# Optimization experiments

Measured on AMD Instinct MI355X. Metric: run time of the kernel, lower is better.

The kernel has to match this reference:

```python
import jax, jax.numpy as jnp
import numpy as np

N = 30000        # nodes
E = 480000       # edges
IN_DIM = 128
HID = 64
OUT = 64
POS_DIM = 32
H = 4            # heads (same for all layers)
PVOCAB = 3
NEG_SLOPE = 0.2


def _xavier(key, shape):
    fan_in, fan_out = shape[0], shape[-1] if len(shape) > 1 else shape[0]
    scale = 1.414 * np.sqrt(2.0 / (fan_in + fan_out))
    return jax.random.normal(key, shape, dtype=jnp.float32) * scale


def setup_inputs() -> dict:
    key = jax.random.key(0)
    ks = jax.random.split(key, 20)
    d0_in = IN_DIM + POS_DIM            # 160
    d_mid = HID * H + POS_DIM           # 288
    inp = {
        "features": jax.random.normal(ks[0], (N, IN_DIM), dtype=jnp.float32),
        # layer 0
        "W0": _xavier(ks[1], (d0_in, H * HID)),
        "al0": _xavier(ks[2], (H, HID)),
        "ar0": _xavier(ks[3], (H, HID)),
        "pe0": _xavier(ks[4], (PVOCAB, POS_DIM)),
        # layer 1
        "W1": _xavier(ks[5], (d_mid, H * HID)),
        "al1": _xavier(ks[6], (H, HID)),
        "ar1": _xavier(ks[7], (H, HID)),
        "pe1": _xavier(ks[8], (PVOCAB, POS_DIM)),
        # output layer
        "W2": _xavier(ks[9], (d_mid, H * OUT)),
        "al2": _xavier(ks[10], (H, OUT)),
        "ar2": _xavier(ks[11], (H, OUT)),
        "pe2": _xavier(ks[12], (PVOCAB, POS_DIM)),
        # graph
        "src": jax.random.randint(ks[13], (E,), 0, N, dtype=jnp.int32),
        "dst": jax.random.randint(ks[14], (E,), 0, N, dtype=jnp.int32),
        "pos": jax.random.randint(ks[15], (N,), 0, PVOCAB, dtype=jnp.int32),
    }
    return inp


def gat_layer(h, W, a_l, a_r, src, dst):
    # h: [N, in_d]; W: [in_d, H*d]; a_l,a_r: [H, d]
    n = h.shape[0]
    nh, d = a_l.shape
    ft = (h @ W).reshape(n, nh, d)                       # [N,H,d]
    a1 = jnp.einsum("nhd,hd->nh", ft, a_l)               # [N,H]
    a2 = jnp.einsum("nhd,hd->nh", ft, a_r)               # [N,H]
    e = jax.nn.leaky_relu(a1[src] + a2[dst], NEG_SLOPE)  # [E,H]
    # per-destination segment softmax (numerically stable)
    m = jax.ops.segment_max(e, dst, num_segments=n)      # [N,H]
    ex = jnp.exp(e - m[dst])                             # [E,H]
    s = jax.ops.segment_sum(ex, dst, num_segments=n)     # [N,H]
    alpha = ex / s[dst]                                  # [E,H]
    msg = ft[src] * alpha[:, :, None]                    # [E,H,d]
    return jax.ops.segment_sum(msg, dst, num_segments=n) # [N,H,d]


def reference(features, W0, al0, ar0, pe0, W1, al1, ar1, pe1,
              W2, al2, ar2, pe2, src, dst, pos):
    h = features
    # hidden GAT layers with ELU activation and head-flattening
    for W, al, ar, pe in ((W0, al0, ar0, pe0), (W1, al1, ar1, pe1)):
        p = pe[pos]                                      # [N, pos_dim]
        hcat = jnp.concatenate((h, p), axis=1)
        out = gat_layer(hcat, W, al, ar, src, dst)       # [N,H,d]
        h = jax.nn.elu(out.reshape(out.shape[0], -1))    # [N,H*d]
    # output layer: mean over heads
    p = pe2[pos]
    hcat = jnp.concatenate((h, p), axis=1)
    out = gat_layer(hcat, W2, al2, ar2, src, dst)        # [N,H,out]
    return out.mean(axis=1)                              # [N,out]
```

## Files before the change

### kernel.cpp

```cpp
#include <hip/hip_runtime.h>
#include <hip/hip_fp16.h>
#include <math.h>

#define N_NODES 30000
#define N_EDGES 480000
#define HEADS 4
#define DHEAD 64
#define FDIM 256
#define POSD 32
#define CAPB 96
#define HIST_NB 1875
#define G0_NB 940

typedef _Float16 half8 __attribute__((ext_vector_type(8)));
typedef float floatx4 __attribute__((ext_vector_type(4)));

__device__ __forceinline__ float lrelu(float x){ return x > 0.f ? x : 0.2f * x; }

struct h16 { __half2 a, b, c, d; };
union hu { half8 v; h16 s; };

template<typename T>
__device__ __forceinline__ void gemm_body(
    int bx, int by, const T* __restrict__ A, const _Float16* __restrict__ Wt,
    const float* __restrict__ PW, const int* __restrict__ pos,
    const float* __restrict__ al, const float* __restrict__ arw,
    _Float16* __restrict__ Ch, float* __restrict__ a1, float* __restrict__ a2,
    int K){
  int t = threadIdx.x;
  int w = t >> 6;
  int lane = t & 63;
  int lm = lane & 15;
  int kq = lane >> 4;
  int h = bx;
  int rowBase = by * 128 + w * 32;
  int colBase = h * DHEAD;

  floatx4 acc[2][4] = {};

  const T* Ar[2];
#pragma unroll
  for (int r = 0; r < 2; r++)
    Ar[r] = A + (size_t)min(rowBase + r * 16 + lm, N_NODES - 1) * K;
  const _Float16* Bp[4];
#pragma unroll
  for (int j = 0; j < 4; j++)
    Bp[j] = Wt + (size_t)(colBase + j * 16 + lm) * K;

  for (int kb = 0; kb < K; kb += 32){
    int ko = kb + kq * 8;
    half8 bf[4];
#pragma unroll
    for (int j = 0; j < 4; j++) bf[j] = *(const half8*)(Bp[j] + ko);
#pragma unroll
    for (int r = 0; r < 2; r++){
      half8 af;
      if constexpr (sizeof(T) == 2){
        af = *(const half8*)(Ar[r] + ko);
      } else {
        float4 u0 = *(const float4*)(Ar[r] + ko);
        float4 u1 = *(const float4*)(Ar[r] + ko + 4);
        af[0] = (_Float16)u0.x; af[1] = (_Float16)u0.y;
        af[2] = (_Float16)u0.z; af[3] = (_Float16)u0.w;
        af[4] = (_Float16)u1.x; af[5] = (_Float16)u1.y;
        af[6] = (_Float16)u1.z; af[7] = (_Float16)u1.w;
      }
#pragma unroll
      for (int j = 0; j < 4; j++)
        acc[r][j] = __builtin_amdgcn_mfma_f32_16x16x32_f16(af, bf[j], acc[r][j], 0, 0, 0);
    }
  }

  float alw[4], arr[4];
#pragma unroll
  for (int j = 0; j < 4; j++){
    int col = j * 16 + lm;
    alw[j] = al [h * DHEAD + col];
    arr[j] = arw[h * DHEAD + col];
  }

#pragma unroll
  for (int r = 0; r < 2; r++){
#pragma unroll
    for (int p = 0; p < 4; p++){
      int row = rowBase + r * 16 + kq * 4 + p;
      if (row < N_NODES){
        int pz = pos[row];
        const float* pwb = PW + pz * FDIM + colBase;
        float s1 = 0.f, s2 = 0.f;
#pragma unroll
        for (int j = 0; j < 4; j++){
          float v = acc[r][j][p] + pwb[j * 16 + lm];
          Ch[(size_t)row * FDIM + colBase + j * 16 + lm] = (_Float16)v;
          s1 = fmaf(v, alw[j], s1);
          s2 = fmaf(v, arr[j], s2);
        }
#pragma unroll
        for (int o2 = 1; o2 <= 8; o2 <<= 1){
          s1 += __shfl_xor(s1, o2, 64);
          s2 += __shfl_xor(s2, o2, 64);
        }
        if (lm == 0){
          a1[row * HEADS + h] = s1;
          a2[row * HEADS + h] = s2;
        }
      }
    }
  }
}

__device__ __forceinline__ void pair_batch(
    const _Float16* __restrict__ ftp, int sr, float wr, int base,
    int eh, int hh, float4& aL, float4& aH){
  int s4[4]; float w4[4]; hu f4[4];
#pragma unroll
  for (int u = 0; u < 4; u++){
    int eu = base + 2 * u + eh;
    s4[u] = __shfl(sr, eu, 64);
    w4[u] = __shfl(wr, eu | (hh << 4), 64);
  }
#pragma unroll
  for (int u = 0; u < 4; u++)
    f4[u].v = *(const half8*)(ftp + (size_t)s4[u] * FDIM);
#pragma unroll
  for (int u = 0; u < 4; u++){
    float2 p0 = __half22float2(f4[u].s.a);
    float2 p1 = __half22float2(f4[u].s.b);
    float2 p2 = __half22float2(f4[u].s.c);
    float2 p3 = __half22float2(f4[u].s.d);
    float wu = w4[u];
    aL.x = fmaf(wu, p0.x, aL.x); aL.y = fmaf(wu, p0.y, aL.y);
    aL.z = fmaf(wu, p1.x, aL.z); aL.w = fmaf(wu, p1.y, aL.w);
    aH.x = fmaf(wu, p2.x, aH.x); aH.y = fmaf(wu, p2.y, aH.y);
    aH.z = fmaf(wu, p3.x, aH.z); aH.w = fmaf(wu, p3.y, aH.w);
  }
}

__device__ __forceinline__ void agg_node(
    int n, const _Float16* __restrict__ ft, const float* __restrict__ a1,
    const float* __restrict__ a2, const int* __restrict__ degv,
    const int* __restrict__ esrc, int lane, float4& aL, float4& aH){
  int jb = n * CAPB;
  int deg = min(degv[n], CAPB);
  int eidx = lane & 15, h = lane >> 4;
  int eh = lane >> 5;
  int c8 = lane & 31;
  int hh = (lane >> 3) & 3;
  float a2n = a2[n * HEADS + h];
  aL = make_float4(0.f, 0.f, 0.f, 0.f);
  aH = make_float4(0.f, 0.f, 0.f, 0.f);
  const _Float16* ftp = ft + (size_t)c8 * 8;

  if (deg <= 64){
    int sreg[4];
#pragma unroll
    for (int r = 0; r < 4; r++){
      int idx = eidx + r * 16;
      sreg[r] = (idx < deg) ? esrc[jb + idx] : 0;
    }
    float av[4];
#pragma unroll
    for (int r = 0; r < 4; r++)
      av[r] = a1[sreg[r] * HEADS + h];
    int sA[4]; hu fA[4];
#pragma unroll
    for (int u = 0; u < 4; u++) sA[u] = __shfl(sreg[0], 2 * u + eh, 64);
#pragma unroll
    for (int u = 0; u < 4; u++)
      fA[u].v = *(const half8*)(ftp + (size_t)sA[u] * FDIM);

    float wreg[4];
    float m = -INFINITY;
#pragma unroll
    for (int r = 0; r < 4; r++){
      int idx = eidx + r * 16;
      float e = (idx < deg) ? lrelu(av[r] + a2n) : -INFINITY;
      wreg[r] = e;
      m = fmaxf(m, e);
    }
    m = fmaxf(m, __shfl_xor(m, 1, 64));
    m = fmaxf(m, __shfl_xor(m, 2, 64));
    m = fmaxf(m, __shfl_xor(m, 4, 64));
    m = fmaxf(m, __shfl_xor(m, 8, 64));
    float ss = 0.f;
#pragma unroll
    for (int r = 0; r < 4; r++){
      int idx = eidx + r * 16;
      float tv = (idx < deg) ? __expf(wreg[r] - m) : 0.f;
      wreg[r] = tv;
      ss += tv;
    }
    ss += __shfl_xor(ss, 1, 64);
    ss += __shfl_xor(ss, 2, 64);
    ss += __shfl_xor(ss, 4, 64);
    ss += __shfl_xor(ss, 8, 64);
    float inv = (ss > 0.f) ? 1.f / ss : 0.f;
#pragma unroll
    for (int r = 0; r < 4; r++) wreg[r] *= inv;

    {
      float w4[4];
#pragma unroll
      for (int u = 0; u < 4; u++)
        w4[u] = __shfl(wreg[0], (2 * u + eh) | (hh << 4), 64);
#pragma unroll
      for (int u = 0; u < 4; u++){
        float2 p0 = __half22float2(fA[u].s.a);
        float2 p1 = __half22float2(fA[u].s.b);
        float2 p2 = __half22float2(fA[u].s.c);
        float2 p3 = __half22float2(fA[u].s.d);
        float wu = w4[u];
        aL.x = fmaf(wu, p0.x, aL.x); aL.y = fmaf(wu, p0.y, aL.y);
        aL.z = fmaf(wu, p1.x, aL.z); aL.w = fmaf(wu, p1.y, aL.w);
        aH.x = fmaf(wu, p2.x, aH.x); aH.y = fmaf(wu, p2.y, aH.y);
        aH.z = fmaf(wu, p3.x, aH.z); aH.w = fmaf(wu, p3.y, aH.w);
      }
    }
    if (deg > 8)
      pair_batch(ftp, sreg[0], wreg[0], 8, eh, hh, aL, aH);
#pragma unroll
    for (int r = 1; r < 4; r++){
      if (r * 16 >= deg) break;
      pair_batch(ftp, sreg[r], wreg[r], 0, eh, hh, aL, aH);
      if (deg > r * 16 + 8)
        pair_batch(ftp, sreg[r], wreg[r], 8, eh, hh, aL, aH);
    }
  } else {
    float m = -INFINITY;
    for (int idx = eidx; idx < deg; idx += 16){
      int s = esrc[jb + idx];
      m = fmaxf(m, lrelu(a1[s * HEADS + h] + a2n));
    }
    m = fmaxf(m, __shfl_xor(m, 1, 64));
    m = fmaxf(m, __shfl_xor(m, 2, 64));
    m = fmaxf(m, __shfl_xor(m, 4, 64));
    m = fmaxf(m, __shfl_xor(m, 8, 64));
    float ss = 0.f;
    for (int idx = eidx; idx < deg; idx += 16){
      int s = esrc[jb + idx];
      ss += __expf(lrelu(a1[s * HEADS + h] + a2n) - m);
    }
    ss += __shfl_xor(ss, 1, 64);
    ss += __shfl_xor(ss, 2, 64);
    ss += __shfl_xor(ss, 4, 64);
    ss += __shfl_xor(ss, 8, 64);
    float inv = (ss > 0.f) ? 1.f / ss : 0.f;
    float m2  = __shfl(m,   hh << 4, 64);
    float iv2 = __shfl(inv, hh << 4, 64);
    float a2h = __shfl(a2n, hh << 4, 64);
    for (int j = eh; j < deg; j += 2){
      int sj = esrc[jb + j];
      float e = lrelu(a1[sj * HEADS + hh] + a2h);
      float wj = __expf(e - m2) * iv2;
      hu f; f.v = *(const half8*)(ftp + (size_t)sj * FDIM);
      float2 p0 = __half22float2(f.s.a);
      float2 p1 = __half22float2(f.s.b);
      float2 p2 = __half22float2(f.s.c);
      float2 p3 = __half22float2(f.s.d);
      aL.x = fmaf(wj, p0.x, aL.x); aL.y = fmaf(wj, p0.y, aL.y);
      aL.z = fmaf(wj, p1.x, aL.z); aL.w = fmaf(wj, p1.y, aL.w);
      aH.x = fmaf(wj, p2.x, aH.x); aH.y = fmaf(wj, p2.y, aH.y);
      aH.z = fmaf(wj, p3.x, aH.z); aH.w = fmaf(wj, p3.y, aH.w);
    }
  }
}

__global__ __launch_bounds__(256) void agg4_k(
    const _Float16* __restrict__ ft, const float* __restrict__ a1,
    const float* __restrict__ a2, const int* __restrict__ degv,
    const int* __restrict__ esrc, _Float16* __restrict__ outh,
    float* __restrict__ outf, int mode){
  int wv = threadIdx.x >> 6;
  int lane = threadIdx.x & 63;
  int n = blockIdx.x * 4 + wv;
  if (n >= N_NODES) return;
  float4 aL, aH;
  agg_node(n, ft, a1, a2, degv, esrc, lane, aL, aH);

  aL.x += __shfl_xor(aL.x, 32, 64); aL.y += __shfl_xor(aL.y, 32, 64);
  aL.z += __shfl_xor(aL.z, 32, 64); aL.w += __shfl_xor(aL.w, 32, 64);
  aH.x += __shfl_xor(aH.x, 32, 64); aH.y += __shfl_xor(aH.y, 32, 64);
  aH.z += __shfl_xor(aH.z, 32, 64); aH.w += __shfl_xor(aH.w, 32, 64);

  if (mode == 0){
    aL.x = aL.x > 0.f ? aL.x : (__expf(aL.x) - 1.f);
    aL.y = aL.y > 0.f ? aL.y : (__expf(aL.y) - 1.f);
    aL.z = aL.z > 0.f ? aL.z : (__expf(aL.z) - 1.f);
    aL.w = aL.w > 0.f ? aL.w : (__expf(aL.w) - 1.f);
    aH.x = aH.x > 0.f ? aH.x : (__expf(aH.x) - 1.f);
    aH.y = aH.y > 0.f ? aH.y : (__expf(aH.y) - 1.f);
    aH.z = aH.z > 0.f ? aH.z : (__expf(aH.z) - 1.f);
    aH.w = aH.w > 0.f ? aH.w : (__expf(aH.w) - 1.f);
    if (lane < 32){
      h16 o;
      o.a = __float22half2_rn(make_float2(aL.x, aL.y));
      o.b = __float22half2_rn(make_float2(aL.z, aL.w));
      o.c = __float22half2_rn(make_float2(aH.x, aH.y));
      o.d = __float22half2_rn(make_float2(aH.z, aH.w));
      *(h16*)&outh[(size_t)n * FDIM + (size_t)lane * 8] = o;
    }
  } else {
#pragma unroll
    for (int o2 = 8; o2 <= 16; o2 <<= 1){
      aL.x += __shfl_xor(aL.x, o2, 64); aL.y += __shfl_xor(aL.y, o2, 64);
      aL.z += __shfl_xor(aL.z, o2, 64); aL.w += __shfl_xor(aL.w, o2, 64);
      aH.x += __shfl_xor(aH.x, o2, 64); aH.y += __shfl_xor(aH.y, o2, 64);
      aH.z += __shfl_xor(aH.z, o2, 64); aH.w += __shfl_xor(aH.w, o2, 64);
    }
    if (lane < 8){
      float4 o0 = make_float4(aL.x * 0.25f, aL.y * 0.25f,
                              aL.z * 0.25f, aL.w * 0.25f);
      float4 o1 = make_float4(aH.x * 0.25f, aH.y * 0.25f,
                              aH.z * 0.25f, aH.w * 0.25f);
      *(float4*)&outf[(size_t)n * DHEAD + (size_t)lane * 8]     = o0;
      *(float4*)&outf[(size_t)n * DHEAD + (size_t)lane * 8 + 4] = o1;
    }
  }
}

__global__ __launch_bounds__(256) void prep0_k(
    const float* __restrict__ W0, const float* __restrict__ pe0,
    _Float16* __restrict__ T0, float* __restrict__ PW, int* __restrict__ deg){
  int blk = blockIdx.x, n = threadIdx.x;
  if (blk < 64){
    for (int k = blk; k < 128; k += 64)
      T0[(size_t)n * 128 + k] = (_Float16)W0[(size_t)k * FDIM + n];
  } else if (blk < 67){
    int v = blk - 64;
    float s = 0.f;
#pragma unroll
    for (int k = 0; k < POSD; k++)
      s = fmaf(pe0[v * POSD + k], W0[(size_t)(128 + k) * FDIM + n], s);
    PW[v * FDIM + n] = s;
  } else {
    int i = (blk - 67) * 256 + n;
    if (i < N_NODES) deg[i] = 0;
  }
}

__global__ __launch_bounds__(256, 2) void fused0_k(
    const float* __restrict__ A, const _Float16* __restrict__ Wt0,
    const float* __restrict__ PW0, const int* __restrict__ pos,
    const float* __restrict__ al0, const float* __restrict__ ar0,
    _Float16* __restrict__ Ch, float* __restrict__ a1, float* __restrict__ a2,
    const int* __restrict__ src, const int* __restrict__ dst,
    int* __restrict__ deg, int* __restrict__ esrc,
    const float* __restrict__ W1, const float* __restrict__ W2,
    _Float16* __restrict__ T1, _Float16* __restrict__ T2,
    const float* __restrict__ pe1, const float* __restrict__ pe2,
    float* __restrict__ PWall){
  int blk = blockIdx.x;
  if (blk < G0_NB){
    gemm_body<float>(blk & 3, blk >> 2, A, Wt0, PW0, pos, al0, ar0,
                     Ch, a1, a2, 128);
  } else if (blk < G0_NB + HIST_NB){
    int e = (blk - G0_NB) * 256 + threadIdx.x;
    if (e < N_EDGES){
      int d = dst[e];
      int slot = atomicAdd(&deg[d], 1);
      if (slot < CAPB) esrc[d * CAPB + slot] = src[e];
    }
  } else if (blk < G0_NB + HIST_NB + 128){
    int q = blk - G0_NB - HIST_NB;
    int l = q >> 6, kk0 = q & 63;
    const float* W = l == 0 ? W1 : W2;
    _Float16* T    = l == 0 ? T1 : T2;
    int n = threadIdx.x;
    for (int k = kk0; k < 256; k += 64)
      T[(size_t)n * 256 + k] = (_Float16)W[(size_t)k * FDIM + n];
  } else {
    int q = blk - G0_NB - HIST_NB - 128;
    int layer = q / 3 + 1, v = q % 3;
    const float* W  = layer == 1 ? W1 : W2;
    const float* pe = layer == 1 ? pe1 : pe2;
    int j = threadIdx.x;
    float s = 0.f;
#pragma unroll
    for (int k = 0; k < POSD; k++)
      s = fmaf(pe[v * POSD + k], W[(size_t)(256 + k) * FDIM + j], s);
    PWall[(layer * 3 + v) * FDIM + j] = s;
  }
}

template<typename T>
__global__ __launch_bounds__(256, 2) void gemm_k(
    const T* __restrict__ A, const _Float16* __restrict__ Wt,
    const float* __restrict__ PW, const int* __restrict__ pos,
    const float* __restrict__ al, const float* __restrict__ arw,
    _Float16* __restrict__ Ch, float* __restrict__ a1, float* __restrict__ a2,
    int K){
  gemm_body<T>(blockIdx.x, blockIdx.y, A, Wt, PW, pos, al, arw, Ch, a1, a2, K);
}

extern "C" void kernel_launch(void* const* d_in, const int* in_sizes, int n_in,
                              void* d_out, int out_size, void* d_ws, size_t ws_size,
                              hipStream_t stream){
  const float* features = (const float*)d_in[0];
  const float* W0  = (const float*)d_in[1];
  const float* al0 = (const float*)d_in[2];
  const float* ar0 = (const float*)d_in[3];
  const float* pe0 = (const float*)d_in[4];
  const float* W1  = (const float*)d_in[5];
  const float* al1 = (const float*)d_in[6];
  const float* ar1 = (const float*)d_in[7];
  const float* pe1 = (const float*)d_in[8];
  const float* W2  = (const float*)d_in[9];
  const float* al2 = (const float*)d_in[10];
  const float* ar2 = (const float*)d_in[11];
  const float* pe2 = (const float*)d_in[12];
  const int* srcv  = (const int*)d_in[13];
  const int* dstv  = (const int*)d_in[14];
  const int* posv  = (const int*)d_in[15];
  float* out = (float*)d_out;

  char* wp = (char*)d_ws;
  auto alloc = [&](size_t bytes){
    void* q = (void*)wp;
    wp += (bytes + 255) & ~(size_t)255;
    return q;
  };
  _Float16* fth  = (_Float16*)alloc(sizeof(_Float16) * (size_t)N_NODES * FDIM);
  _Float16* hbuf = (_Float16*)alloc(sizeof(_Float16) * (size_t)N_NODES * FDIM);
  _Float16* Wt0  = (_Float16*)alloc(sizeof(_Float16) * 256 * 128);
  _Float16* Wt1  = (_Float16*)alloc(sizeof(_Float16) * 256 * 256);
  _Float16* Wt2  = (_Float16*)alloc(sizeof(_Float16) * 256 * 256);
  float* a1   = (float*)alloc(sizeof(float) * N_NODES * HEADS);
  float* a2   = (float*)alloc(sizeof(float) * N_NODES * HEADS);
  float* PW   = (float*)alloc(sizeof(float) * 9 * FDIM);
  int*   deg  = (int*)alloc(sizeof(int) * N_NODES);
  int*   esrc = (int*)alloc(sizeof(int) * (size_t)N_NODES * CAPB);

  prep0_k<<<185, 256, 0, stream>>>(W0, pe0, Wt0, PW, deg);

  fused0_k<<<G0_NB + HIST_NB + 134, 256, 0, stream>>>(
      features, Wt0, PW, posv, al0, ar0, fth, a1, a2,
      srcv, dstv, deg, esrc, W1, W2, Wt1, Wt2, pe1, pe2, PW);

  dim3 ggrid(4, (N_NODES + 127) / 128);
  int agrid = (N_NODES + 3) / 4;

  agg4_k<<<agrid, 256, 0, stream>>>(fth, a1, a2, deg, esrc, hbuf, nullptr, 0);

  gemm_k<_Float16><<<ggrid, 256, 0, stream>>>(
      hbuf, Wt1, PW + 3 * FDIM, posv, al1, ar1, fth, a1, a2, 256);
  agg4_k<<<agrid, 256, 0, stream>>>(fth, a1, a2, deg, esrc, hbuf, nullptr, 0);

  gemm_k<_Float16><<<ggrid, 256, 0, stream>>>(
      hbuf, Wt2, PW + 6 * FDIM, posv, al2, ar2, fth, a1, a2, 256);
  agg4_k<<<agrid, 256, 0, stream>>>(fth, a1, a2, deg, esrc, nullptr, out, 1);
}
```

Baseline: 284.2 us.

## Fuse hidden-layer aggregation with next layer's GEMM through shared memory

```diff
diff --git a/kernel.cpp b/kernel.cpp
--- a/kernel.cpp
+++ b/kernel.cpp
@@ -11,6 +11,7 @@
 #define CAPB 96
 #define HIST_NB 1875
 #define G0_NB 940
+#define LDS_STRIDE 264
 
 typedef _Float16 half8 __attribute__((ext_vector_type(8)));
 typedef float floatx4 __attribute__((ext_vector_type(4)));
@@ -265,11 +266,121 @@
   }
 }
 
+__global__ __launch_bounds__(256) void aggemm32_k(
+    const _Float16* __restrict__ ftin, const float* __restrict__ a1in,
+    const float* __restrict__ a2in, const int* __restrict__ degv,
+    const int* __restrict__ esrc, const _Float16* __restrict__ Wt,
+    const float* __restrict__ PW, const int* __restrict__ pos,
+    const float* __restrict__ al, const float* __restrict__ arw,
+    _Float16* __restrict__ ftout, float* __restrict__ a1out,
+    float* __restrict__ a2out){
+  __shared__ _Float16 As[32 * LDS_STRIDE];
+  int t = threadIdx.x;
+  int wv = t >> 6;
+  int lane = t & 63;
+  int rb = blockIdx.x * 32;
+
+  for (int i = 0; i < 8; i++){
+    int rl = wv * 8 + i;
+    int n = rb + rl;
+    float4 aL = make_float4(0.f, 0.f, 0.f, 0.f);
+    float4 aH = make_float4(0.f, 0.f, 0.f, 0.f);
+    if (n < N_NODES){
+      agg_node(n, ftin, a1in, a2in, degv, esrc, lane, aL, aH);
+      aL.x += __shfl_xor(aL.x, 32, 64); aL.y += __shfl_xor(aL.y, 32, 64);
+      aL.z += __shfl_xor(aL.z, 32, 64); aL.w += __shfl_xor(aL.w, 32, 64);
+      aH.x += __shfl_xor(aH.x, 32, 64); aH.y += __shfl_xor(aH.y, 32, 64);
+      aH.z += __shfl_xor(aH.z, 32, 64); aH.w += __shfl_xor(aH.w, 32, 64);
+      aL.x = aL.x > 0.f ? aL.x : (__expf(aL.x) - 1.f);
+      aL.y = aL.y > 0.f ? aL.y : (__expf(aL.y) - 1.f);
+      aL.z = aL.z > 0.f ? aL.z : (__expf(aL.z) - 1.f);
+      aL.w = aL.w > 0.f ? aL.w : (__expf(aL.w) - 1.f);
+      aH.x = aH.x > 0.f ? aH.x : (__expf(aH.x) - 1.f);
+      aH.y = aH.y > 0.f ? aH.y : (__expf(aH.y) - 1.f);
+      aH.z = aH.z > 0.f ? aH.z : (__expf(aH.z) - 1.f);
+      aH.w = aH.w > 0.f ? aH.w : (__expf(aH.w) - 1.f);
+    }
+    if (lane < 32){
+      h16 o;
+      o.a = __float22half2_rn(make_float2(aL.x, aL.y));
+      o.b = __float22half2_rn(make_float2(aL.z, aL.w));
+      o.c = __float22half2_rn(make_float2(aH.x, aH.y));
+      o.d = __float22half2_rn(make_float2(aH.z, aH.w));
+      *(h16*)&As[rl * LDS_STRIDE + lane * 8] = o;
+    }
+  }
+  __syncthreads();
+
+  int lm = lane & 15;
+  int kq = lane >> 4;
+  int colBase = wv * DHEAD;
+
+  floatx4 acc[2][4] = {};
+  const _Float16* Arl[2];
+#pragma unroll
+  for (int r = 0; r < 2; r++)
+    Arl[r] = As + (r * 16 + lm) * LDS_STRIDE;
+  const _Float16* Bp[4];
+#pragma unroll
+  for (int j = 0; j < 4; j++)
+    Bp[j] = Wt + (size_t)(colBase + j * 16 + lm) * 256;
+
+  for (int kb = 0; kb < 256; kb += 32){
+    int ko = kb + kq * 8;
+    half8 bf[4];
+#pragma unroll
+    for (int j = 0; j < 4; j++) bf[j] = *(const half8*)(Bp[j] + ko);
+#pragma unroll
+    for (int r = 0; r < 2; r++){
+      half8 af = *(const half8*)(Arl[r] + ko);
+#pragma unroll
+      for (int j = 0; j < 4; j++)
+        acc[r][j] = __builtin_amdgcn_mfma_f32_16x16x32_f16(af, bf[j], acc[r][j], 0, 0, 0);
+    }
+  }
+
+  float alw[4], arr[4];
+#pragma unroll
+  for (int j = 0; j < 4; j++){
+    int col = j * 16 + lm;
+    alw[j] = al [wv * DHEAD + col];
+    arr[j] = arw[wv * DHEAD + col];
+  }
+
+#pragma unroll
+  for (int r = 0; r < 2; r++){
+#pragma unroll
+    for (int p = 0; p < 4; p++){
+      int row = rb + r * 16 + kq * 4 + p;
+      if (row < N_NODES){
+        int pz = pos[row];
+        const float* pwb = PW + pz * FDIM + colBase;
+        float s1 = 0.f, s2 = 0.f;
+#pragma unroll
+        for (int j = 0; j < 4; j++){
+          float v = acc[r][j][p] + pwb[j * 16 + lm];
+          ftout[(size_t)row * FDIM + colBase + j * 16 + lm] = (_Float16)v;
+          s1 = fmaf(v, alw[j], s1);
+          s2 = fmaf(v, arr[j], s2);
+        }
+#pragma unroll
+        for (int o2 = 1; o2 <= 8; o2 <<= 1){
+          s1 += __shfl_xor(s1, o2, 64);
+          s2 += __shfl_xor(s2, o2, 64);
+        }
+        if (lm == 0){
+          a1out[row * HEADS + wv] = s1;
+          a2out[row * HEADS + wv] = s2;
+        }
+      }
+    }
+  }
+}
+
 __global__ __launch_bounds__(256) void agg4_k(
     const _Float16* __restrict__ ft, const float* __restrict__ a1,
     const float* __restrict__ a2, const int* __restrict__ degv,
-    const int* __restrict__ esrc, _Float16* __restrict__ outh,
-    float* __restrict__ outf, int mode){
+    const int* __restrict__ esrc, float* __restrict__ outf){
   int wv = threadIdx.x >> 6;
   int lane = threadIdx.x & 63;
   int n = blockIdx.x * 4 + wv;
@@ -282,39 +393,20 @@
   aH.x += __shfl_xor(aH.x, 32, 64); aH.y += __shfl_xor(aH.y, 32, 64);
   aH.z += __shfl_xor(aH.z, 32, 64); aH.w += __shfl_xor(aH.w, 32, 64);
 
-  if (mode == 0){
-    aL.x = aL.x > 0.f ? aL.x : (__expf(aL.x) - 1.f);
-    aL.y = aL.y > 0.f ? aL.y : (__expf(aL.y) - 1.f);
-    aL.z = aL.z > 0.f ? aL.z : (__expf(aL.z) - 1.f);
-    aL.w = aL.w > 0.f ? aL.w : (__expf(aL.w) - 1.f);
-    aH.x = aH.x > 0.f ? aH.x : (__expf(aH.x) - 1.f);
-    aH.y = aH.y > 0.f ? aH.y : (__expf(aH.y) - 1.f);
-    aH.z = aH.z > 0.f ? aH.z : (__expf(aH.z) - 1.f);
-    aH.w = aH.w > 0.f ? aH.w : (__expf(aH.w) - 1.f);
-    if (lane < 32){
-      h16 o;
-      o.a = __float22half2_rn(make_float2(aL.x, aL.y));
-      o.b = __float22half2_rn(make_float2(aL.z, aL.w));
-      o.c = __float22half2_rn(make_float2(aH.x, aH.y));
-      o.d = __float22half2_rn(make_float2(aH.z, aH.w));
-      *(h16*)&outh[(size_t)n * FDIM + (size_t)lane * 8] = o;
-    }
-  } else {
-#pragma unroll
-    for (int o2 = 8; o2 <= 16; o2 <<= 1){
-      aL.x += __shfl_xor(aL.x, o2, 64); aL.y += __shfl_xor(aL.y, o2, 64);
-      aL.z += __shfl_xor(aL.z, o2, 64); aL.w += __shfl_xor(aL.w, o2, 64);
-      aH.x += __shfl_xor(aH.x, o2, 64); aH.y += __shfl_xor(aH.y, o2, 64);
-      aH.z += __shfl_xor(aH.z, o2, 64); aH.w += __shfl_xor(aH.w, o2, 64);
-    }
-    if (lane < 8){
-      float4 o0 = make_float4(aL.x * 0.25f, aL.y * 0.25f,
-                              aL.z * 0.25f, aL.w * 0.25f);
-      float4 o1 = make_float4(aH.x * 0.25f, aH.y * 0.25f,
-                              aH.z * 0.25f, aH.w * 0.25f);
-      *(float4*)&outf[(size_t)n * DHEAD + (size_t)lane * 8]     = o0;
-      *(float4*)&outf[(size_t)n * DHEAD + (size_t)lane * 8 + 4] = o1;
-    }
+#pragma unroll
+  for (int o2 = 8; o2 <= 16; o2 <<= 1){
+    aL.x += __shfl_xor(aL.x, o2, 64); aL.y += __shfl_xor(aL.y, o2, 64);
+    aL.z += __shfl_xor(aL.z, o2, 64); aL.w += __shfl_xor(aL.w, o2, 64);
+    aH.x += __shfl_xor(aH.x, o2, 64); aH.y += __shfl_xor(aH.y, o2, 64);
+    aH.z += __shfl_xor(aH.z, o2, 64); aH.w += __shfl_xor(aH.w, o2, 64);
+  }
+  if (lane < 8){
+    float4 o0 = make_float4(aL.x * 0.25f, aL.y * 0.25f,
+                            aL.z * 0.25f, aL.w * 0.25f);
+    float4 o1 = make_float4(aH.x * 0.25f, aH.y * 0.25f,
+                            aH.z * 0.25f, aH.w * 0.25f);
+    *(float4*)&outf[(size_t)n * DHEAD + (size_t)lane * 8]     = o0;
+    *(float4*)&outf[(size_t)n * DHEAD + (size_t)lane * 8 + 4] = o1;
   }
 }
 
@@ -382,16 +474,6 @@
   }
 }
 
-template<typename T>
-__global__ __launch_bounds__(256, 2) void gemm_k(
-    const T* __restrict__ A, const _Float16* __restrict__ Wt,
-    const float* __restrict__ PW, const int* __restrict__ pos,
-    const float* __restrict__ al, const float* __restrict__ arw,
-    _Float16* __restrict__ Ch, float* __restrict__ a1, float* __restrict__ a2,
-    int K){
-  gemm_body<T>(blockIdx.x, blockIdx.y, A, Wt, PW, pos, al, arw, Ch, a1, a2, K);
-}
-
 extern "C" void kernel_launch(void* const* d_in, const int* in_sizes, int n_in,
                               void* d_out, int out_size, void* d_ws, size_t ws_size,
                               hipStream_t stream){
@@ -419,33 +501,33 @@
     wp += (bytes + 255) & ~(size_t)255;
     return q;
   };
-  _Float16* fth  = (_Float16*)alloc(sizeof(_Float16) * (size_t)N_NODES * FDIM);
-  _Float16* hbuf = (_Float16*)alloc(sizeof(_Float16) * (size_t)N_NODES * FDIM);
-  _Float16* Wt0  = (_Float16*)alloc(sizeof(_Float16) * 256 * 128);
-  _Float16* Wt1  = (_Float16*)alloc(sizeof(_Float16) * 256 * 256);
-  _Float16* Wt2  = (_Float16*)alloc(sizeof(_Float16) * 256 * 256);
-  float* a1   = (float*)alloc(sizeof(float) * N_NODES * HEADS);
-  float* a2   = (float*)alloc(sizeof(float) * N_NODES * HEADS);
-  float* PW   = (float*)alloc(sizeof(float) * 9 * FDIM);
-  int*   deg  = (int*)alloc(sizeof(int) * N_NODES);
-  int*   esrc = (int*)alloc(sizeof(int) * (size_t)N_NODES * CAPB);
+  _Float16* F0  = (_Float16*)alloc(sizeof(_Float16) * (size_t)N_NODES * FDIM);
+  _Float16* F1  = (_Float16*)alloc(sizeof(_Float16) * (size_t)N_NODES * FDIM);
+  _Float16* Wt0 = (_Float16*)alloc(sizeof(_Float16) * 256 * 128);
+  _Float16* Wt1 = (_Float16*)alloc(sizeof(_Float16) * 256 * 256);
+  _Float16* Wt2 = (_Float16*)alloc(sizeof(_Float16) * 256 * 256);
+  float* a1A = (float*)alloc(sizeof(float) * N_NODES * HEADS);
+  float* a2A = (float*)alloc(sizeof(float) * N_NODES * HEADS);
+  float* a1B = (float*)alloc(sizeof(float) * N_NODES * HEADS);
+  float* a2B = (float*)alloc(sizeof(float) * N_NODES * HEADS);
+  float* PW  = (float*)alloc(sizeof(float) * 9 * FDIM);
+  int*   deg = (int*)alloc(sizeof(int) * N_NODES);
+  int*   esrc= (int*)alloc(sizeof(int) * (size_t)N_NODES * CAPB);
 
   prep0_k<<<185, 256, 0, stream>>>(W0, pe0, Wt0, PW, deg);
 
   fused0_k<<<G0_NB + HIST_NB + 134, 256, 0, stream>>>(
-      features, Wt0, PW, posv, al0, ar0, fth, a1, a2,
+      features, Wt0, PW, posv, al0, ar0, F0, a1A, a2A,
       srcv, dstv, deg, esrc, W1, W2, Wt1, Wt2, pe1, pe2, PW);
 
-  dim3 ggrid(4, (N_NODES + 127) / 128);
-  int agrid = (N_NODES + 3) / 4;
-
-  agg4_k<<<agrid, 256, 0, stream>>>(fth, a1, a2, deg, esrc, hbuf, nullptr, 0);
-
-  gemm_k<_Float16><<<ggrid, 256, 0, stream>>>(
-      hbuf, Wt1, PW + 3 * FDIM, posv, al1, ar1, fth, a1, a2, 256);
-  agg4_k<<<agrid, 256, 0, stream>>>(fth, a1, a2, deg, esrc, hbuf, nullptr, 0);
-
-  gemm_k<_Float16><<<ggrid, 256, 0, stream>>>(
-      hbuf, Wt2, PW + 6 * FDIM, posv, al2, ar2, fth, a1, a2, 256);
-  agg4_k<<<agrid, 256, 0, stream>>>(fth, a1, a2, deg, esrc, nullptr, out, 1);
-}
+  aggemm32_k<<<(N_NODES + 31) / 32, 256, 0, stream>>>(
+      F0, a1A, a2A, deg, esrc, Wt1, PW + 3 * FDIM, posv, al1, ar1,
+      F1, a1B, a2B);
+
+  aggemm32_k<<<(N_NODES + 31) / 32, 256, 0, stream>>>(
+      F1, a1B, a2B, deg, esrc, Wt2, PW + 6 * FDIM, posv, al2, ar2,
+      F0, a1A, a2A);
+
+  agg4_k<<<(N_NODES + 3) / 4, 256, 0, stream>>>(
+      F0, a1A, a2A, deg, esrc, out);
+}
```

New measurement: 302.8 us. +6.6%, slower.
